# Kernel optimization log

Hardware: AMD Instinct MI355X
Metric: run time of the kernel (lower is better)

The kernel has to match this reference:

```python
import jax, jax.numpy as jnp
import numpy as np

B, C, L = 2, 2048, 8192  # batch, channels = d_model*(order-1), seq_len


def setup_inputs() -> dict:
    key = jax.random.key(0)
    k1, k2, k3 = jax.random.split(key, 3)
    x = jax.random.normal(k1, (B, C, L), dtype=jnp.float32)
    # implicit long-conv filter produced by HyenaFilter, materialized as a learned tensor
    k = jax.random.normal(k2, (C, L), dtype=jnp.float32) * 0.02
    bias = jax.random.normal(k3, (C,), dtype=jnp.float32)
    return {"x": x, "k": k, "bias": bias}


def reference(x, k, bias):
    # FFT-based causal depthwise long convolution (Hyena fftconv):
    #   y[b,c,t] = sum_{s<=t} k[c,s] * x[b,c,t-s]  + bias[c] * x[b,c,t]
    L_ = x.shape[-1]
    fft_size = 2 * L_  # zero-pad to 2L for linear (non-circular) convolution
    k_f = jnp.fft.rfft(k, n=fft_size) / fft_size          # [C, fft/2+1] complex
    x_f = jnp.fft.rfft(x, n=fft_size)                     # [B, C, fft/2+1]
    y = jnp.fft.irfft(x_f * k_f, n=fft_size, norm="forward")[..., :L_]
    return y + x * bias[None, :, None]
```

## Files before the change

### kernel.cpp

```cpp
#include <hip/hip_runtime.h>

#define LSEQ 8192
#define NFFT 8192
#define NT2 512
#define CCH 2048
#define TWO_PI 6.283185307179586f
#define PI_F  3.14159265358979323846f
#define KSTRIDE 8208

__device__ __forceinline__ int SL2(int i) { return i ^ (((i >> 4) & 15) << 1); }

__device__ __forceinline__ float2 cmul(float2 a, float2 b) {
    return b * a.x + make_float2(-b.y, b.x) * a.y;
}
__device__ __forceinline__ float2 conjf2(float2 a) { return make_float2(a.x, -a.y); }

template<int SGN>
__device__ __forceinline__ float2 muli(float2 t) {
    return (SGN < 0) ? make_float2(t.y, -t.x) : make_float2(-t.y, t.x);
}

template<int SGN>
__device__ __forceinline__ void dft4(float2& a0, float2& a1, float2& a2, float2& a3) {
    float2 t0 = a0 + a2, t1 = a0 - a2, t2 = a1 + a3, t3 = a1 - a3;
    float2 u = muli<SGN>(t3);
    a0 = t0 + t2; a1 = t1 + u; a2 = t0 - t2; a3 = t1 - u;
}

template<int SGN>
__device__ __forceinline__ void dft8(float2& v0, float2& v1, float2& v2, float2& v3,
                                     float2& v4, float2& v5, float2& v6, float2& v7) {
    float2 e0 = v0, e1 = v2, e2 = v4, e3 = v6;
    float2 o0 = v1, o1 = v3, o2 = v5, o3 = v7;
    dft4<SGN>(e0, e1, e2, e3);
    dft4<SGN>(o0, o1, o2, o3);
    const float sg = (float)SGN;
    const float H = 0.7071067811865476f;
    float2 t1 = cmul(o1, make_float2( H, sg * H));
    float2 t2 = muli<SGN>(o2);
    float2 t3 = cmul(o3, make_float2(-H, sg * H));
    v0 = e0 + o0; v4 = e0 - o0;
    v1 = e1 + t1; v5 = e1 - t1;
    v2 = e2 + t2; v6 = e2 - t2;
    v3 = e3 + t3; v7 = e3 - t3;
}

__device__ __forceinline__ void rdr(const float2* p, float2& lo, float2& hi) {
    const float4 v = *reinterpret_cast<const float4*>(p);
    lo = make_float2(v.x, v.y);
    hi = make_float2(v.z, v.w);
}
__device__ __forceinline__ void wrr(float2* p, float2 lo, float2 hi) {
    *reinterpret_cast<float4*>(p) = make_float4(lo.x, lo.y, hi.x, hi.y);
}
__device__ __forceinline__ void wrp(float2* ds, int e, float2 lo, float2 hi) {
    wrr(&ds[SL2(e)], lo, hi);
}

#define RD8X                                                                  \
    float2 a0,a1,a2,a3,a4,a5,a6,a7,b0,b1,b2,b3,b4,b5,b6,b7;                   \
    {   const float2* p_ = ds + SL2(B_);                                      \
        rdr(p_,        a0, b0);                                               \
        rdr(p_ + 1024, a1, b1);                                               \
        rdr(p_ + 2048, a2, b2);                                               \
        rdr(p_ + 3072, a3, b3);                                               \
        rdr(p_ + 4096, a4, b4);                                               \
        rdr(p_ + 5120, a5, b5);                                               \
        rdr(p_ + 6144, a6, b6);                                               \
        rdr(p_ + 7168, a7, b7);                                               \
    }

#define DFT8AB(SGN)                                                           \
    dft8<(SGN)>(a0,a1,a2,a3,a4,a5,a6,a7);                                     \
    dft8<(SGN)>(b0,b1,b2,b3,b4,b5,b6,b7);

#define TWID(SGN, NSv, WDC, WDS) {                                            \
    float s_, c_;                                                             \
    __sincosf((float)(SGN) * TWO_PI / (float)((NSv) * 8) *                    \
              (float)(B_ & ((NSv) - 1)), &s_, &c_);                           \
    const float2 w1a = make_float2(c_, s_);                                   \
    a1 = cmul(a1, w1a);                                                       \
    const float2 w2a = cmul(w1a, w1a);                                        \
    a2 = cmul(a2, w2a);                                                       \
    const float2 w3a = cmul(w2a, w1a);                                        \
    a3 = cmul(a3, w3a);                                                       \
    const float2 w4a = cmul(w2a, w2a);                                        \
    a4 = cmul(a4, w4a);                                                       \
    a5 = cmul(a5, cmul(w3a, w2a));                                            \
    a6 = cmul(a6, cmul(w3a, w3a));                                            \
    a7 = cmul(a7, cmul(w4a, w3a));                                            \
    const float2 w1b = cmul(w1a, make_float2((WDC), (float)(SGN) * (WDS)));   \
    b1 = cmul(b1, w1b);                                                       \
    const float2 w2b = cmul(w1b, w1b);                                        \
    b2 = cmul(b2, w2b);                                                       \
    const float2 w3b = cmul(w2b, w1b);                                        \
    b3 = cmul(b3, w3b);                                                       \
    const float2 w4b = cmul(w2b, w2b);                                        \
    b4 = cmul(b4, w4b);                                                       \
    b5 = cmul(b5, cmul(w3b, w2b));                                            \
    b6 = cmul(b6, cmul(w3b, w3b));                                            \
    b7 = cmul(b7, cmul(w4b, w3b));                                            \
}

#define WR8P(NSv) {                                                           \
    const int i_ = B_ & ((NSv) - 1);                                          \
    const int d_ = ((B_ - i_) << 3) + i_;                                     \
    wrp(ds, d_,             a0, b0);                                          \
    wrp(ds, d_ +     (NSv), a1, b1);                                          \
    wrp(ds, d_ + 2 * (NSv), a2, b2);                                          \
    wrp(ds, d_ + 3 * (NSv), a3, b3);                                          \
    wrp(ds, d_ + 4 * (NSv), a4, b4);                                          \
    wrp(ds, d_ + 5 * (NSv), a5, b5);                                          \
    wrp(ds, d_ + 6 * (NSv), a6, b6);                                          \
    wrp(ds, d_ + 7 * (NSv), a7, b7);                                          \
}

#define WR8SEQ {                                                              \
    const int d_ = B_ << 3;                                                   \
    wrp(ds, d_,      a0, a1);                                                 \
    wrp(ds, d_ +  2, a2, a3);                                                 \
    wrp(ds, d_ +  4, a4, a5);                                                 \
    wrp(ds, d_ +  6, a6, a7);                                                 \
    wrp(ds, d_ +  8, b0, b1);                                                 \
    wrp(ds, d_ + 10, b2, b3);                                                 \
    wrp(ds, d_ + 12, b4, b5);                                                 \
    wrp(ds, d_ + 14, b6, b7);                                                 \
}

#define P8MID(SGN, NSv, WDC, WDS) {                                           \
    RD8X                                                                      \
    TWID(SGN, NSv, WDC, WDS)                                                  \
    DFT8AB(SGN)                                                               \
    __syncthreads();                                                          \
    WR8P(NSv)                                                                 \
    __syncthreads();                                                          \
}

#define P8FIRST_LDS(SGN) {                                                    \
    RD8X                                                                      \
    DFT8AB(SGN)                                                               \
    __syncthreads();                                                          \
    WR8SEQ                                                                    \
    __syncthreads();                                                          \
}

#define WD8C  0.9951847266721969f
#define WD8S  0.0980171403295606f
#define WD64C 0.9999247018391445f
#define WD64S 0.012271538285719925f

#define DFT16M(SGN, P) {                                                            \
    dft4<(SGN)>(P##0, P##4, P##8,  P##12);                                          \
    dft4<(SGN)>(P##1, P##5, P##9,  P##13);                                          \
    dft4<(SGN)>(P##2, P##6, P##10, P##14);                                          \
    dft4<(SGN)>(P##3, P##7, P##11, P##15);                                          \
    const float sg_ = (float)(SGN);                                                 \
    const float2 tw1_ = make_float2( 0.9238795325112867f,  sg_ * 0.3826834323650898f); \
    const float2 tw2_ = make_float2( 0.7071067811865476f,  sg_ * 0.7071067811865476f); \
    const float2 tw3_ = make_float2( 0.3826834323650898f,  sg_ * 0.9238795325112867f); \
    const float2 tw6_ = make_float2(-0.7071067811865476f,  sg_ * 0.7071067811865476f); \
    const float2 tw9_ = make_float2(-0.9238795325112867f, -sg_ * 0.3826834323650898f); \
    P##5  = cmul(P##5,  tw1_);                                                      \
    P##6  = cmul(P##6,  tw2_);                                                      \
    P##7  = cmul(P##7,  tw3_);                                                      \
    P##9  = cmul(P##9,  tw2_);                                                      \
    P##10 = muli<(SGN)>(P##10);                                                     \
    P##11 = cmul(P##11, tw6_);                                                      \
    P##13 = cmul(P##13, tw3_);                                                      \
    P##14 = cmul(P##14, tw6_);                                                      \
    P##15 = cmul(P##15, tw9_);                                                      \
    dft4<(SGN)>(P##0,  P##1,  P##2,  P##3);                                         \
    dft4<(SGN)>(P##4,  P##5,  P##6,  P##7);                                         \
    dft4<(SGN)>(P##8,  P##9,  P##10, P##11);                                        \
    dft4<(SGN)>(P##12, P##13, P##14, P##15);                                        \
}

#define R16_LOAD_TWIDDLE(SGN)                                                 \
    float2 m0,m1,m2,m3,m4,m5,m6,m7,m8,m9,m10,m11,m12,m13,m14,m15;             \
    {   const float2* p_ = ds + SL2(tid);                                     \
        m0  = p_[0];    m1  = p_[512];  m2  = p_[1024]; m3  = p_[1536];       \
        m4  = p_[2048]; m5  = p_[2560]; m6  = p_[3072]; m7  = p_[3584];       \
        m8  = p_[4096]; m9  = p_[4608]; m10 = p_[5120]; m11 = p_[5632];       \
        m12 = p_[6144]; m13 = p_[6656]; m14 = p_[7168]; m15 = p_[7680];       \
    }                                                                         \
    {   float s_, c_;                                                         \
        __sincosf((float)(SGN) * TWO_PI / 8192.0f * (float)tid, &s_, &c_);    \
        const float2 w1 = make_float2(c_, s_);                                \
        m1 = cmul(m1, w1);                                                    \
        const float2 w2 = cmul(w1, w1);   m2  = cmul(m2,  w2);                \
        const float2 w3 = cmul(w2, w1);   m3  = cmul(m3,  w3);                \
        const float2 w4 = cmul(w2, w2);   m4  = cmul(m4,  w4);                \
        const float2 w5 = cmul(w3, w2);   m5  = cmul(m5,  w5);                \
        const float2 w6 = cmul(w3, w3);   m6  = cmul(m6,  w6);                \
        const float2 w7 = cmul(w4, w3);   m7  = cmul(m7,  w7);                \
        const float2 w8 = cmul(w4, w4);   m8  = cmul(m8,  w8);                \
        m9  = cmul(m9,  cmul(w5, w4));                                        \
        m10 = cmul(m10, cmul(w5, w5));                                        \
        m11 = cmul(m11, cmul(w6, w5));                                        \
        m12 = cmul(m12, cmul(w6, w6));                                        \
        m13 = cmul(m13, cmul(w7, w6));                                        \
        m14 = cmul(m14, cmul(w7, w7));                                        \
        m15 = cmul(m15, cmul(w8, w7));                                        \
    }

#define R16_STORE_LDS {                                                       \
    float2* p_ = ds + SL2(tid);                                               \
    p_[0]    = m0;  p_[512]  = m4;  p_[1024] = m8;  p_[1536] = m12;           \
    p_[2048] = m1;  p_[2560] = m5;  p_[3072] = m9;  p_[3584] = m13;           \
    p_[4096] = m2;  p_[4608] = m6;  p_[5120] = m10; p_[5632] = m14;           \
    p_[6144] = m3;  p_[6656] = m7;  p_[7168] = m11; p_[7680] = m15;           \
}

#define UE1 make_float2(0.9807852804032304f, 0.1950903220161283f)

__global__ __launch_bounds__(NT2)
void hyena_kfft8(const float* __restrict__ k, const float* __restrict__ bias,
                 float2* __restrict__ kw)
{
    __shared__ alignas(16) float2 ds[NFFT];
    const int c = blockIdx.x, tid = threadIdx.x;
    const int B_ = tid << 1;
    const float* kp = k + (size_t)c * LSEQ;
    const float bsv = bias[c];

    {
        float2 a0,a1,a2,a3,a4,a5,a6,a7,b0,b1,b2,b3,b4,b5,b6,b7;
        float4 v;
        v = *(const float4*)&kp[(B_ << 1)];
        a0 = make_float2(v.x, v.y); b0 = make_float2(v.z, v.w);
        if (tid == 0) a0.x += bsv;
        v = *(const float4*)&kp[(B_ << 1) + 2048];
        a1 = make_float2(v.x, v.y); b1 = make_float2(v.z, v.w);
        v = *(const float4*)&kp[(B_ << 1) + 4096];
        a2 = make_float2(v.x, v.y); b2 = make_float2(v.z, v.w);
        v = *(const float4*)&kp[(B_ << 1) + 6144];
        a3 = make_float2(v.x, v.y); b3 = make_float2(v.z, v.w);
        a4 = a5 = a6 = a7 = b4 = b5 = b6 = b7 = make_float2(0.f, 0.f);
        DFT8AB(-1)
        WR8SEQ
        __syncthreads();
    }
    P8MID(-1, 8,  WD8C,  WD8S)
    P8MID(-1, 64, WD64C, WD64S)
    {
        R16_LOAD_TWIDDLE(-1)
        DFT16M(-1, m)
        R16_STORE_LDS
    }
    __syncthreads();

    {
        const float sc = 1.0f / 16384.0f;
        float2* kc = kw + (size_t)c * KSTRIDE;
        float2* pj_ = ds + SL2(tid);
        const int mb_ = (tid == 0) ? 8192 : (7680 + SL2(512 - tid));
        float s0_, c0_;
        __sincosf(PI_F / 8192.0f * (float)tid, &s0_, &c0_);
        float2 cs = make_float2(c0_, s0_);
#pragma unroll
        for (int r = 0; r < 8; r++) {
            if (tid == 0 && r == 0) {
                float2 W0 = ds[SL2(0)];
                kc[0]    = make_float2((W0.x + W0.y) * sc, 0.f);
                kc[8192] = make_float2((W0.x - W0.y) * sc, 0.f);
                float2 W4 = ds[SL2(4096)];
                kc[4096] = make_float2(W4.x * sc, -W4.y * sc);
            } else {
                const int j  = tid + (r << 9);
                const int jm = NFFT - j;
                float2 Wj = pj_[r << 9];
                float2 Wm = ds[mb_ - (r << 9)];
                float2 E = (Wj + conjf2(Wm)) * 0.5f;
                float2 D = (Wj - conjf2(Wm)) * 0.5f;
                float2 O = make_float2(D.y, -D.x);
                const float c_ = cs.x, s_ = cs.y;
                float2 tO = cmul(O, make_float2(c_, -s_));
                float2 uO = cmul(conjf2(O), make_float2(c_, s_));
                kc[j]  = (E + tO) * sc;
                kc[jm] = (conjf2(E) - uO) * sc;
            }
            cs = cmul(cs, UE1);
        }
    }
}

__global__ __launch_bounds__(NT2)
void hyena_xconv8(const float* __restrict__ x, const float2* __restrict__ kw,
                  float* __restrict__ y)
{
    __shared__ alignas(16) float2 ds[NFFT];
    const int bid = blockIdx.x, tid = threadIdx.x;
    const int c = bid >> 1, b = bid & 1;
    const int B_ = tid << 1;
    const float* xp = x + ((size_t)(b * CCH + c)) * LSEQ;
    float*       yp = y + ((size_t)(b * CCH + c)) * LSEQ;

    {
        float2 a0,a1,a2,a3,a4,a5,a6,a7,b0,b1,b2,b3,b4,b5,b6,b7;
        float4 v;
        v = *(const float4*)&xp[(B_ << 1)];
        a0 = make_float2(v.x, v.y); b0 = make_float2(v.z, v.w);
        v = *(const float4*)&xp[(B_ << 1) + 2048];
        a1 = make_float2(v.x, v.y); b1 = make_float2(v.z, v.w);
        v = *(const float4*)&xp[(B_ << 1) + 4096];
        a2 = make_float2(v.x, v.y); b2 = make_float2(v.z, v.w);
        v = *(const float4*)&xp[(B_ << 1) + 6144];
        a3 = make_float2(v.x, v.y); b3 = make_float2(v.z, v.w);
        a4 = a5 = a6 = a7 = b4 = b5 = b6 = b7 = make_float2(0.f, 0.f);
        DFT8AB(-1)
        WR8SEQ
        __syncthreads();
    }
    P8MID(-1, 8,  WD8C,  WD8S)
    P8MID(-1, 64, WD64C, WD64S)
    {
        R16_LOAD_TWIDDLE(-1)
        DFT16M(-1, m)
        R16_STORE_LDS
    }
    __syncthreads();

    {
        const float2* kc = kw + (size_t)c * KSTRIDE;
        float2* pj_ = ds + SL2(tid);
        const int mb_ = (tid == 0) ? 8192 : (7680 + SL2(512 - tid));
        float s0_, c0_;
        __sincosf(PI_F / 8192.0f * (float)tid, &s0_, &c0_);
        float2 cs = make_float2(c0_, s0_);
#pragma unroll
        for (int r = 0; r < 8; r++) {
            if (tid == 0 && r == 0) {
                float2 W0 = ds[SL2(0)];
                float X0 = W0.x + W0.y, XN = W0.x - W0.y;
                float2 K0 = kc[0], KN = kc[8192];
                float2 Z0 = make_float2(X0 * K0.x, X0 * K0.y);
                float2 ZN = make_float2(XN * KN.x, XN * KN.y);
                ds[SL2(0)] = make_float2(Z0.x + ZN.x - (Z0.y - ZN.y),
                                         Z0.y + ZN.y + (Z0.x - ZN.x));
                float2 W4 = ds[SL2(4096)];
                float2 Z4 = cmul(conjf2(W4), kc[4096]);
                ds[SL2(4096)] = make_float2(2.f * Z4.x, -2.f * Z4.y);
            } else {
                const int j  = tid + (r << 9);
                const int jm = NFFT - j;
                float2 Wj = pj_[r << 9];
                float2 Wm = ds[mb_ - (r << 9)];
                float2 E = (Wj + conjf2(Wm)) * 0.5f;
                float2 D = (Wj - conjf2(Wm)) * 0.5f;
                float2 O = make_float2(D.y, -D.x);
                const float c_ = cs.x, s_ = cs.y;
                float2 Xj = E + cmul(O, make_float2(c_, -s_));
                float2 Xm = conjf2(E) - cmul(conjf2(O), make_float2(c_, s_));
                float2 Zj = cmul(Xj, kc[j]);
                float2 Zm = cmul(Xm, kc[jm]);
                float2 P  = Zj + conjf2(Zm);
                float2 Q  = Zj - conjf2(Zm);
                float2 Vj = P + cmul(Q, make_float2(-s_, c_));
                float2 P2 = Zm + conjf2(Zj);
                float2 Q2 = Zm - conjf2(Zj);
                float2 Vm = P2 + cmul(Q2, make_float2(-s_, -c_));
                pj_[r << 9]        = Vj;
                ds[mb_ - (r << 9)] = Vm;
            }
            cs = cmul(cs, UE1);
        }
    }
    __syncthreads();

    P8FIRST_LDS(1)
    P8MID(1, 8,  WD8C,  WD8S)
    P8MID(1, 64, WD64C, WD64S)
    {
        R16_LOAD_TWIDDLE(1)
        DFT16M(1, m)
        *(float2*)&yp[(tid) << 1]          = m0;
        *(float2*)&yp[(tid +  512) << 1]   = m4;
        *(float2*)&yp[(tid + 1024) << 1]   = m8;
        *(float2*)&yp[(tid + 1536) << 1]   = m12;
        *(float2*)&yp[(tid + 2048) << 1]   = m1;
        *(float2*)&yp[(tid + 2560) << 1]   = m5;
        *(float2*)&yp[(tid + 3072) << 1]   = m9;
        *(float2*)&yp[(tid + 3584) << 1]   = m13;
    }
}

extern "C" void kernel_launch(void* const* d_in, const int* in_sizes, int n_in,
                              void* d_out, int out_size, void* d_ws, size_t ws_size,
                              hipStream_t stream) {
    const float* x    = (const float*)d_in[0];
    const float* k    = (const float*)d_in[1];
    const float* bias = (const float*)d_in[2];
    float* y          = (float*)d_out;
    float2* kw        = (float2*)d_ws;

    hyena_kfft8 <<<dim3(CCH),     dim3(NT2), 0, stream>>>(k, bias, kw);
    hyena_xconv8<<<dim3(2 * CCH), dim3(NT2), 0, stream>>>(x, kw, y);
}
```

Before: 182.2 us.

## Fuse spectral multiply into register-resident inverse FFT first stage

```diff
diff --git a/kernel.cpp b/kernel.cpp
--- a/kernel.cpp
+++ b/kernel.cpp
@@ -136,18 +136,16 @@
     __syncthreads();                                                          \
 }
 
-#define P8FIRST_LDS(SGN) {                                                    \
-    RD8X                                                                      \
-    DFT8AB(SGN)                                                               \
-    __syncthreads();                                                          \
-    WR8SEQ                                                                    \
-    __syncthreads();                                                          \
-}
-
-#define WD8C  0.9951847266721969f
-#define WD8S  0.0980171403295606f
-#define WD64C 0.9999247018391445f
-#define WD64S 0.012271538285719925f
+#define WD8C   0.9951847266721969f
+#define WD8S   0.0980171403295606f
+#define WD64C  0.9999247018391445f
+#define WD64S  0.012271538285719925f
+#define WD16C  0.9987954562051724f
+#define WD16S  0.049067674327418015f
+#define WD128C 0.9999811752826011f
+#define WD128S 0.006135884649154475f
+#define WDF_C  0.9999997058628822f
+#define WDF_S  0.0007669903187427045f
 
 #define DFT16M(SGN, P) {                                                            \
     dft4<(SGN)>(P##0, P##4, P##8,  P##12);                                          \
@@ -212,6 +210,21 @@
 }
 
 #define UE1 make_float2(0.9807852804032304f, 0.1950903220161283f)
+
+#define UNT(R, MW, VOUT) {                                                    \
+    float2 Wm_ = ds[mb_ - 512 * (R)];                                         \
+    float2 E_ = (MW + conjf2(Wm_)) * 0.5f;                                    \
+    float2 D_ = (MW - conjf2(Wm_)) * 0.5f;                                    \
+    float2 O_ = make_float2(D_.y, -D_.x);                                     \
+    float2 Xj_ = E_ + cmul(O_, conjf2(cs));                                   \
+    float2 Xm_ = conjf2(E_) - cmul(conjf2(O_), cs);                           \
+    float2 Zj_ = cmul(Xj_, kc[tid + 512 * (R)]);                              \
+    float2 Zm_ = cmul(Xm_, kc[8192 - tid - 512 * (R)]);                       \
+    float2 P_ = Zj_ + conjf2(Zm_);                                            \
+    float2 Q_ = Zj_ - conjf2(Zm_);                                            \
+    VOUT = P_ + cmul(Q_, make_float2(-cs.y, cs.x));                           \
+    cs = cmul(cs, UE1);                                                       \
+}
 
 __global__ __launch_bounds__(NT2)
 void hyena_kfft8(const float* __restrict__ k, const float* __restrict__ bias,
@@ -313,74 +326,72 @@
     }
     P8MID(-1, 8,  WD8C,  WD8S)
     P8MID(-1, 64, WD64C, WD64S)
+
     {
         R16_LOAD_TWIDDLE(-1)
         DFT16M(-1, m)
         R16_STORE_LDS
-    }
-    __syncthreads();
-
-    {
+        __syncthreads();
+
         const float2* kc = kw + (size_t)c * KSTRIDE;
-        float2* pj_ = ds + SL2(tid);
         const int mb_ = (tid == 0) ? 8192 : (7680 + SL2(512 - tid));
         float s0_, c0_;
         __sincosf(PI_F / 8192.0f * (float)tid, &s0_, &c0_);
         float2 cs = make_float2(c0_, s0_);
-#pragma unroll
-        for (int r = 0; r < 8; r++) {
-            if (tid == 0 && r == 0) {
-                float2 W0 = ds[SL2(0)];
-                float X0 = W0.x + W0.y, XN = W0.x - W0.y;
-                float2 K0 = kc[0], KN = kc[8192];
-                float2 Z0 = make_float2(X0 * K0.x, X0 * K0.y);
-                float2 ZN = make_float2(XN * KN.x, XN * KN.y);
-                ds[SL2(0)] = make_float2(Z0.x + ZN.x - (Z0.y - ZN.y),
-                                         Z0.y + ZN.y + (Z0.x - ZN.x));
-                float2 W4 = ds[SL2(4096)];
-                float2 Z4 = cmul(conjf2(W4), kc[4096]);
-                ds[SL2(4096)] = make_float2(2.f * Z4.x, -2.f * Z4.y);
-            } else {
-                const int j  = tid + (r << 9);
-                const int jm = NFFT - j;
-                float2 Wj = pj_[r << 9];
-                float2 Wm = ds[mb_ - (r << 9)];
-                float2 E = (Wj + conjf2(Wm)) * 0.5f;
-                float2 D = (Wj - conjf2(Wm)) * 0.5f;
-                float2 O = make_float2(D.y, -D.x);
-                const float c_ = cs.x, s_ = cs.y;
-                float2 Xj = E + cmul(O, make_float2(c_, -s_));
-                float2 Xm = conjf2(E) - cmul(conjf2(O), make_float2(c_, s_));
-                float2 Zj = cmul(Xj, kc[j]);
-                float2 Zm = cmul(Xm, kc[jm]);
-                float2 P  = Zj + conjf2(Zm);
-                float2 Q  = Zj - conjf2(Zm);
-                float2 Vj = P + cmul(Q, make_float2(-s_, c_));
-                float2 P2 = Zm + conjf2(Zj);
-                float2 Q2 = Zm - conjf2(Zj);
-                float2 Vm = P2 + cmul(Q2, make_float2(-s_, -c_));
-                pj_[r << 9]        = Vj;
-                ds[mb_ - (r << 9)] = Vm;
-            }
+        float2 v0,v1,v2,v3,v4,v5,v6,v7,v8,v9,v10,v11,v12,v13,v14,v15;
+
+        if (tid == 0) {
+            float X0 = m0.x + m0.y, XN = m0.x - m0.y;
+            float2 K0 = kc[0], KN = kc[8192];
+            float2 Z0 = K0 * X0;
+            float2 ZN = KN * XN;
+            v0 = make_float2(Z0.x + ZN.x - (Z0.y - ZN.y),
+                             Z0.y + ZN.y + (Z0.x - ZN.x));
             cs = cmul(cs, UE1);
+        } else {
+            UNT(0, m0, v0)
         }
-    }
-    __syncthreads();
-
-    P8FIRST_LDS(1)
-    P8MID(1, 8,  WD8C,  WD8S)
-    P8MID(1, 64, WD64C, WD64S)
-    {
-        R16_LOAD_TWIDDLE(1)
-        DFT16M(1, m)
-        *(float2*)&yp[(tid) << 1]          = m0;
-        *(float2*)&yp[(tid +  512) << 1]   = m4;
-        *(float2*)&yp[(tid + 1024) << 1]   = m8;
-        *(float2*)&yp[(tid + 1536) << 1]   = m12;
-        *(float2*)&yp[(tid + 2048) << 1]   = m1;
-        *(float2*)&yp[(tid + 2560) << 1]   = m5;
-        *(float2*)&yp[(tid + 3072) << 1]   = m9;
-        *(float2*)&yp[(tid + 3584) << 1]   = m13;
+        UNT(1,  m4,  v1)
+        UNT(2,  m8,  v2)
+        UNT(3,  m12, v3)
+        UNT(4,  m1,  v4)
+        UNT(5,  m5,  v5)
+        UNT(6,  m9,  v6)
+        UNT(7,  m13, v7)
+        UNT(8,  m2,  v8)
+        UNT(9,  m6,  v9)
+        UNT(10, m10, v10)
+        UNT(11, m14, v11)
+        UNT(12, m3,  v12)
+        UNT(13, m7,  v13)
+        UNT(14, m11, v14)
+        UNT(15, m15, v15)
+        __syncthreads();
+
+        DFT16M(1, v)
+        const int d0_ = tid << 4;
+        wrp(ds, d0_,      v0,  v4);
+        wrp(ds, d0_ +  2, v8,  v12);
+        wrp(ds, d0_ +  4, v1,  v5);
+        wrp(ds, d0_ +  6, v9,  v13);
+        wrp(ds, d0_ +  8, v2,  v6);
+        wrp(ds, d0_ + 10, v10, v14);
+        wrp(ds, d0_ + 12, v3,  v7);
+        wrp(ds, d0_ + 14, v11, v15);
+        __syncthreads();
+    }
+
+    P8MID(1, 16,  WD16C,  WD16S)
+    P8MID(1, 128, WD128C, WD128S)
+
+    {
+        RD8X
+        TWID(1, 1024, WDF_C, WDF_S)
+        DFT8AB(1)
+        *(float4*)&yp[(B_) << 1]        = make_float4(a0.x, a0.y, b0.x, b0.y);
+        *(float4*)&yp[(B_ + 1024) << 1] = make_float4(a1.x, a1.y, b1.x, b1.y);
+        *(float4*)&yp[(B_ + 2048) << 1] = make_float4(a2.x, a2.y, b2.x, b2.y);
+        *(float4*)&yp[(B_ + 3072) << 1] = make_float4(a3.x, a3.y, b3.x, b3.y);
     }
 }
 
```

Result: slower. 193.7 us (+6.3%).
